# Optimization experiments

Measured on AMD Instinct MI355X. Metric: run time of the kernel, lower is better.

## Reference

```python
import jax, jax.numpy as jnp
import numpy as np


def setup_inputs() -> dict:
    key = jax.random.key(0)
    k1, k2, k3 = jax.random.split(key, 3)
    backbone_feature = jax.random.normal(k1, (8, 256), dtype=jnp.float32)
    grouping_result = jax.random.randint(k2, (8,), 0, 32, dtype=jnp.int64)
    feature = jax.random.normal(k3, (8, 32, 48, 48, 48), dtype=jnp.float32)
    return {"backbone_feature": backbone_feature,
            "grouping_result": grouping_result,
            "feature": feature}


def reference(backbone_feature, grouping_result, feature):
    # feature: [B, R, W, H, D]
    B, R, W, H, D = feature.shape
    dt = feature.dtype
    mgr = feature.mean()  # global mean over all samples/regions/voxels

    # --- per-region argmax position (first occurrence, matching strict '>' scan) ---
    flat = feature.reshape(B, R, W * H * D)
    am = jnp.argmax(flat, axis=-1)                      # [B, R]
    max_x = (am // (H * D)).astype(dt)                  # [B, R]
    max_y = ((am // D) % H).astype(dt)
    max_z = (am % D).astype(dt)

    i = jnp.arange(W, dtype=dt).reshape(1, 1, W, 1, 1)
    j = jnp.arange(H, dtype=dt).reshape(1, 1, 1, H, 1)
    k = jnp.arange(D, dtype=dt).reshape(1, 1, 1, 1, D)

    dx2 = (max_x[:, :, None, None, None] - i) ** 2      # [B,R,W,1,1]
    dy2 = (max_y[:, :, None, None, None] - j) ** 2      # [B,R,1,H,1]
    dz2 = (max_z[:, :, None, None, None] - k) ** 2      # [B,R,1,1,D]

    f2 = feature * feature
    # NOTE: faithful to original parenthesization: z-term is NOT weighted by region^2
    dis_loss = jnp.sum(f2 * (dx2 + dy2)) + jnp.sum(jnp.broadcast_to(dz2, (B, R, W, H, D)))

    # --- exclude-self max over regions via top-2 along region axis ---
    srt = jnp.sort(feature, axis=1)                     # ascending along R
    m1 = srt[:, -1]                                     # [B, W, H, D] max over regions
    m2 = srt[:, -2]                                     # second max
    argmax_r = jnp.argmax(feature, axis=1)              # [B, W, H, D] first-occurrence
    r_ids = jnp.arange(R).reshape(1, R, 1, 1, 1)
    max_others = jnp.where(r_ids == argmax_r[:, None], m2[:, None], m1[:, None])  # [B,R,W,H,D]

    div_loss = jnp.sum(f2 * (max_others - mgr) ** 2)

    sum_num = B * R * W * H * D
    return (jnp.reshape(dis_loss / sum_num, (1,)),
            jnp.reshape(div_loss / sum_num, (1,)))
```

## Files before the change

kernel.cpp:

```cpp
#include <hip/hip_runtime.h>
#include <math.h>

#define W48 48
#define HD 2304
#define WHD 110592
#define NR 32
#define NB 8
#define QPP 27648
#define CHUNKS 108
#define MAIN_BLOCKS 864
#define PARTS 432
#define NTOT 28311552.0

struct PPart { float s0, sx, sy; unsigned int fkey; unsigned int idx; };

__device__ __forceinline__ unsigned fkey_of(float f) {
  unsigned u = __float_as_uint(f);
  return (u & 0x80000000u) ? ~u : (u | 0x80000000u);
}

__device__ __forceinline__ float wave_red_add(float x) {
  int s;
  s = __builtin_amdgcn_update_dpp(0, __float_as_int(x), 0x111, 0xf, 0xf, true); x += __int_as_float(s);
  s = __builtin_amdgcn_update_dpp(0, __float_as_int(x), 0x112, 0xf, 0xf, true); x += __int_as_float(s);
  s = __builtin_amdgcn_update_dpp(0, __float_as_int(x), 0x114, 0xf, 0xf, true); x += __int_as_float(s);
  s = __builtin_amdgcn_update_dpp(0, __float_as_int(x), 0x118, 0xf, 0xf, true); x += __int_as_float(s);
  s = __builtin_amdgcn_update_dpp(0, __float_as_int(x), 0x142, 0xa, 0xf, true); x += __int_as_float(s);
  s = __builtin_amdgcn_update_dpp(0, __float_as_int(x), 0x143, 0xc, 0xf, true); x += __int_as_float(s);
  return x;
}
__device__ __forceinline__ unsigned wave_red_umax(unsigned x) {
  int s; unsigned u;
  s = __builtin_amdgcn_update_dpp(0, (int)x, 0x111, 0xf, 0xf, true); u = (unsigned)s; x = x > u ? x : u;
  s = __builtin_amdgcn_update_dpp(0, (int)x, 0x112, 0xf, 0xf, true); u = (unsigned)s; x = x > u ? x : u;
  s = __builtin_amdgcn_update_dpp(0, (int)x, 0x114, 0xf, 0xf, true); u = (unsigned)s; x = x > u ? x : u;
  s = __builtin_amdgcn_update_dpp(0, (int)x, 0x118, 0xf, 0xf, true); u = (unsigned)s; x = x > u ? x : u;
  s = __builtin_amdgcn_update_dpp(0, (int)x, 0x142, 0xa, 0xf, true); u = (unsigned)s; x = x > u ? x : u;
  s = __builtin_amdgcn_update_dpp(0, (int)x, 0x143, 0xc, 0xf, true); u = (unsigned)s; x = x > u ? x : u;
  return x;
}
__device__ __forceinline__ unsigned wave_red_umin(unsigned x) {
  int s; unsigned u;
  s = __builtin_amdgcn_update_dpp(-1, (int)x, 0x111, 0xf, 0xf, false); u = (unsigned)s; x = x < u ? x : u;
  s = __builtin_amdgcn_update_dpp(-1, (int)x, 0x112, 0xf, 0xf, false); u = (unsigned)s; x = x < u ? x : u;
  s = __builtin_amdgcn_update_dpp(-1, (int)x, 0x114, 0xf, 0xf, false); u = (unsigned)s; x = x < u ? x : u;
  s = __builtin_amdgcn_update_dpp(-1, (int)x, 0x118, 0xf, 0xf, false); u = (unsigned)s; x = x < u ? x : u;
  s = __builtin_amdgcn_update_dpp(-1, (int)x, 0x142, 0xa, 0xf, false); u = (unsigned)s; x = x < u ? x : u;
  s = __builtin_amdgcn_update_dpp(-1, (int)x, 0x143, 0xc, 0xf, false); u = (unsigned)s; x = x < u ? x : u;
  return x;
}

__global__ __launch_bounds__(256)
void k_main(const float* __restrict__ feat, PPart* __restrict__ pp,
            double* __restrict__ blk) {
  const int bid = blockIdx.x;
  const int t = threadIdx.x;
  const int b = bid / CHUNKS;
  const int chunk = bid - b * CHUNKS;
  const int qbase = chunk * 256 + t;
  const float4* gbase = reinterpret_cast<const float4*>(feat) + (size_t)b * (NR * QPP) + qbase;

  const int p0 = qbase * 4;
  const int i = p0 / HD;
  const int j = (p0 / W48) % W48;
  const float fi = (float)i, fj = (float)j;
  const float rr = fi * fi + fj * fj;

  const int wave = t >> 6, lane = t & 63;

  float v1[4], v2[4], cp[4];
#pragma unroll
  for (int c = 0; c < 4; ++c) { v1[c] = -INFINITY; v2[c] = -INFINITY; cp[c] = 0.f; }
  float ssum = 0.f, sii = 0.f;

  float4 b0 = gbase[0];
  float4 b1 = gbase[QPP];

#pragma unroll 2
  for (int r = 0; r < NR; ++r) {
    float4 v = b0;
    b0 = b1;
    if (r < NR - 2) b1 = gbase[(size_t)(r + 2) * QPP];

    float vv[4] = {v.x, v.y, v.z, v.w};
    float s0t = 0.f;
#pragma unroll
    for (int c = 0; c < 4; ++c) {
      float f = vv[c];
      float f2 = f * f;
      s0t += f2;
      cp[c] += f2;
      ssum += f;
      float nv2 = fmaxf(f, v2[c]);
      v2[c] = (f > v1[c]) ? v1[c] : nv2;
      v1[c] = fmaxf(v1[c], f);
    }
    float mv = vv[0]; int mc = 0;
#pragma unroll
    for (int c = 1; c < 4; ++c) { if (vv[c] > mv) { mv = vv[c]; mc = c; } }

    sii += s0t * rr;
    float rsx = wave_red_add(s0t * fi);
    float rsy = wave_red_add(s0t * fj);
    float rs0 = wave_red_add(s0t);
    unsigned key = fkey_of(mv);
    unsigned wmax = wave_red_umax(key);
    wmax = (unsigned)__builtin_amdgcn_readlane((int)wmax, 63);
    unsigned cand = (key == wmax) ? (unsigned)(p0 + mc) : 0xffffffffu;
    unsigned widx = wave_red_umin(cand);

    if (lane == 63) {
      PPart o; o.s0 = rs0; o.sx = rsx; o.sy = rsy; o.fkey = wmax; o.idx = widx;
      pp[((size_t)(b * NR + r) * CHUNKS + chunk) * 4 + wave] = o;
    }
  }

  float A = 0.f, Bs = 0.f, C = 0.f;
#pragma unroll
  for (int c = 0; c < 4; ++c) {
    float m1 = v1[c];
    float m1sq = m1 * m1;
    float rest = cp[c] - m1sq;
    A  += m1sq * rest + v2[c] * v2[c] * m1sq;
    Bs += m1 * rest + v2[c] * m1sq;
    C  += cp[c];
  }
  double dA = A, dB = Bs, dC = C, dS = ssum, dI = sii;
#pragma unroll
  for (int off = 32; off; off >>= 1) {
    dA += __shfl_down(dA, off);
    dB += __shfl_down(dB, off);
    dC += __shfl_down(dC, off);
    dS += __shfl_down(dS, off);
    dI += __shfl_down(dI, off);
  }
  __shared__ double ld[4][5];
  if (lane == 0) { ld[wave][0]=dA; ld[wave][1]=dB; ld[wave][2]=dC; ld[wave][3]=dS; ld[wave][4]=dI; }
  __syncthreads();
  if (t == 0) {
    double a=0, bb=0, cc=0, ss=0, si=0;
#pragma unroll
    for (int w = 0; w < 4; ++w) { a+=ld[w][0]; bb+=ld[w][1]; cc+=ld[w][2]; ss+=ld[w][3]; si+=ld[w][4]; }
    blk[(size_t)bid*5+0]=a; blk[(size_t)bid*5+1]=bb; blk[(size_t)bid*5+2]=cc;
    blk[(size_t)bid*5+3]=ss; blk[(size_t)bid*5+4]=si;
  }
}

__global__ __launch_bounds__(512)
void k_planes(const PPart* __restrict__ pp, double* __restrict__ planeDis) {
  const int p = blockIdx.x;
  const int t = threadIdx.x;
  double s0 = 0, sx = 0, sy = 0;
  unsigned fkey = 0, idx = 0xffffffffu;
  if (t < PARTS) {
    PPart v = pp[(size_t)p * PARTS + t];
    s0 = v.s0; sx = v.sx; sy = v.sy; fkey = v.fkey; idx = v.idx;
  }
#pragma unroll
  for (int off = 32; off; off >>= 1) {
    s0 += __shfl_down(s0, off);
    sx += __shfl_down(sx, off);
    sy += __shfl_down(sy, off);
    unsigned ok = __shfl_down(fkey, off);
    unsigned oi = __shfl_down(idx, off);
    if (ok > fkey || (ok == fkey && oi < idx)) { fkey = ok; idx = oi; }
  }
  __shared__ double ls[8][3];
  __shared__ unsigned lk[8][2];
  const int wave = t >> 6, lane = t & 63;
  if (lane == 0) { ls[wave][0]=s0; ls[wave][1]=sx; ls[wave][2]=sy; lk[wave][0]=fkey; lk[wave][1]=idx; }
  __syncthreads();
  if (t == 0) {
    double a0=0, a1=0, a2=0; unsigned bk=0, bi=0xffffffffu;
#pragma unroll
    for (int w = 0; w < 8; ++w) {
      a0 += ls[w][0]; a1 += ls[w][1]; a2 += ls[w][2];
      if (lk[w][0] > bk || (lk[w][0]==bk && lk[w][1] < bi)) { bk = lk[w][0]; bi = lk[w][1]; }
    }
    int am = (int)bi;
    int mx = am / HD;
    int rem = am - mx * HD;
    int my = rem / W48;
    int mz = rem - my * W48;
    double dmx = mx, dmy = my, dmz = mz;
    planeDis[p] = (dmx*dmx + dmy*dmy) * a0 - 2.0*dmx*a1 - 2.0*dmy*a2
                + 2304.0 * (48.0*dmz*dmz - 2256.0*dmz + 35720.0);
  }
}

__global__ __launch_bounds__(256)
void k_fin(const double* __restrict__ planeDis, const double* __restrict__ blk,
           float* __restrict__ out) {
  const int t = threadIdx.x;
  double dis = planeDis[t];
  double A = 0, B = 0, C = 0, S = 0, SII = 0;
  for (int i = t; i < MAIN_BLOCKS; i += 256) {
    A   += blk[(size_t)i*5+0];
    B   += blk[(size_t)i*5+1];
    C   += blk[(size_t)i*5+2];
    S   += blk[(size_t)i*5+3];
    SII += blk[(size_t)i*5+4];
  }
#pragma unroll
  for (int off = 32; off; off >>= 1) {
    dis += __shfl_down(dis, off);
    A   += __shfl_down(A, off);
    B   += __shfl_down(B, off);
    C   += __shfl_down(C, off);
    S   += __shfl_down(S, off);
    SII += __shfl_down(SII, off);
  }
  __shared__ double ls[4][6];
  const int wave = t >> 6, lane = t & 63;
  if (lane == 0) {
    ls[wave][0]=dis; ls[wave][1]=A; ls[wave][2]=B; ls[wave][3]=C; ls[wave][4]=S; ls[wave][5]=SII;
  }
  __syncthreads();
  if (t == 0) {
    double td=0, tA=0, tB=0, tC=0, tS=0, tI=0;
#pragma unroll
    for (int w = 0; w < 4; ++w) {
      td+=ls[w][0]; tA+=ls[w][1]; tB+=ls[w][2]; tC+=ls[w][3]; tS+=ls[w][4]; tI+=ls[w][5];
    }
    double mgr = tS / NTOT;
    out[0] = (float)((td + tI) / NTOT);
    out[1] = (float)((tA - 2.0*mgr*tB + mgr*mgr*tC) / NTOT);
  }
}

extern "C" void kernel_launch(void* const* d_in, const int* in_sizes, int n_in,
                              void* d_out, int out_size, void* d_ws, size_t ws_size,
                              hipStream_t stream) {
  const float* feat = (const float*)d_in[2];
  float* out = (float*)d_out;

  PPart* pp = (PPart*)d_ws;
  double* blk = (double*)((char*)d_ws + 2211840);
  double* planeDis = (double*)((char*)d_ws + 2211840 + 34560);

  k_main<<<MAIN_BLOCKS, 256, 0, stream>>>(feat, pp, blk);
  k_planes<<<256, 512, 0, stream>>>(pp, planeDis);
  k_fin<<<1, 256, 0, stream>>>(planeDis, blk, out);
}
```

Before: 43.63 us.

## Replace per-region DPP wave reductions with batched LDS transpose reduction

Instead of running five DPP wave reductions for every region in every wave, each thread stores its per-region sum of squares and argmax key into LDS. Every 16 regions the block transposes and reduces them, so each thread handles one region over 16 rows. Per-block partials drop from four per wave to one per chunk, which shrinks the partial buffer and lets k_planes use 128-thread blocks. In exchange it uses about 36KB of LDS, which can lower occupancy, and adds barriers inside the fully unrolled region loop.

```diff
diff --git a/kernel.cpp b/kernel.cpp
--- a/kernel.cpp
+++ b/kernel.cpp
@@ -9,123 +9,127 @@
 #define QPP 27648
 #define CHUNKS 108
 #define MAIN_BLOCKS 864
-#define PARTS 432
 #define NTOT 28311552.0
 
-struct PPart { float s0, sx, sy; unsigned int fkey; unsigned int idx; };
-
-__device__ __forceinline__ unsigned fkey_of(float f) {
-  unsigned u = __float_as_uint(f);
-  return (u & 0x80000000u) ? ~u : (u | 0x80000000u);
-}
-
-__device__ __forceinline__ float wave_red_add(float x) {
-  int s;
-  s = __builtin_amdgcn_update_dpp(0, __float_as_int(x), 0x111, 0xf, 0xf, true); x += __int_as_float(s);
-  s = __builtin_amdgcn_update_dpp(0, __float_as_int(x), 0x112, 0xf, 0xf, true); x += __int_as_float(s);
-  s = __builtin_amdgcn_update_dpp(0, __float_as_int(x), 0x114, 0xf, 0xf, true); x += __int_as_float(s);
-  s = __builtin_amdgcn_update_dpp(0, __float_as_int(x), 0x118, 0xf, 0xf, true); x += __int_as_float(s);
-  s = __builtin_amdgcn_update_dpp(0, __float_as_int(x), 0x142, 0xa, 0xf, true); x += __int_as_float(s);
-  s = __builtin_amdgcn_update_dpp(0, __float_as_int(x), 0x143, 0xc, 0xf, true); x += __int_as_float(s);
-  return x;
-}
-__device__ __forceinline__ unsigned wave_red_umax(unsigned x) {
-  int s; unsigned u;
-  s = __builtin_amdgcn_update_dpp(0, (int)x, 0x111, 0xf, 0xf, true); u = (unsigned)s; x = x > u ? x : u;
-  s = __builtin_amdgcn_update_dpp(0, (int)x, 0x112, 0xf, 0xf, true); u = (unsigned)s; x = x > u ? x : u;
-  s = __builtin_amdgcn_update_dpp(0, (int)x, 0x114, 0xf, 0xf, true); u = (unsigned)s; x = x > u ? x : u;
-  s = __builtin_amdgcn_update_dpp(0, (int)x, 0x118, 0xf, 0xf, true); u = (unsigned)s; x = x > u ? x : u;
-  s = __builtin_amdgcn_update_dpp(0, (int)x, 0x142, 0xa, 0xf, true); u = (unsigned)s; x = x > u ? x : u;
-  s = __builtin_amdgcn_update_dpp(0, (int)x, 0x143, 0xc, 0xf, true); u = (unsigned)s; x = x > u ? x : u;
-  return x;
-}
-__device__ __forceinline__ unsigned wave_red_umin(unsigned x) {
-  int s; unsigned u;
-  s = __builtin_amdgcn_update_dpp(-1, (int)x, 0x111, 0xf, 0xf, false); u = (unsigned)s; x = x < u ? x : u;
-  s = __builtin_amdgcn_update_dpp(-1, (int)x, 0x112, 0xf, 0xf, false); u = (unsigned)s; x = x < u ? x : u;
-  s = __builtin_amdgcn_update_dpp(-1, (int)x, 0x114, 0xf, 0xf, false); u = (unsigned)s; x = x < u ? x : u;
-  s = __builtin_amdgcn_update_dpp(-1, (int)x, 0x118, 0xf, 0xf, false); u = (unsigned)s; x = x < u ? x : u;
-  s = __builtin_amdgcn_update_dpp(-1, (int)x, 0x142, 0xa, 0xf, false); u = (unsigned)s; x = x < u ? x : u;
-  s = __builtin_amdgcn_update_dpp(-1, (int)x, 0x143, 0xc, 0xf, false); u = (unsigned)s; x = x < u ? x : u;
-  return x;
-}
+struct PPart { float s0, sx, sy; unsigned key; unsigned idx; };
 
 __global__ __launch_bounds__(256)
 void k_main(const float* __restrict__ feat, PPart* __restrict__ pp,
             double* __restrict__ blk) {
+  __shared__ float    lds_s0[16 * 256];
+  __shared__ unsigned lds_key[16 * 256];
+  __shared__ unsigned lds_mc[256];
+  __shared__ float comb_s0[256], comb_sx[256], comb_sy[256];
+  __shared__ unsigned comb_key[256], comb_idx[256];
+  __shared__ double ld[4][5];
+
   const int bid = blockIdx.x;
   const int t = threadIdx.x;
   const int b = bid / CHUNKS;
   const int chunk = bid - b * CHUNKS;
   const int qbase = chunk * 256 + t;
-  const float4* gbase = reinterpret_cast<const float4*>(feat) + (size_t)b * (NR * QPP) + qbase;
+  const float4* gptr = reinterpret_cast<const float4*>(feat) + (size_t)b * (NR * QPP) + qbase;
 
   const int p0 = qbase * 4;
-  const int i = p0 / HD;
-  const int j = (p0 / W48) % W48;
-  const float fi = (float)i, fj = (float)j;
-  const float rr = fi * fi + fj * fj;
-
-  const int wave = t >> 6, lane = t & 63;
+  const float fi = (float)(p0 / HD);
+  const float fj = (float)((p0 / W48) % W48);
+  const float rrq = fi * fi + fj * fj;
 
   float v1[4], v2[4], cp[4];
 #pragma unroll
   for (int c = 0; c < 4; ++c) { v1[c] = -INFINITY; v2[c] = -INFINITY; cp[c] = 0.f; }
   float ssum = 0.f, sii = 0.f;
-
-  float4 b0 = gbase[0];
-  float4 b1 = gbase[QPP];
-
-#pragma unroll 2
+  unsigned mcpack = 0u;
+
+  float4 nb0 = gptr[0];
+  float4 nb1 = gptr[QPP];
+
+#pragma unroll
   for (int r = 0; r < NR; ++r) {
-    float4 v = b0;
-    b0 = b1;
-    if (r < NR - 2) b1 = gbase[(size_t)(r + 2) * QPP];
+    float4 v = nb0; nb0 = nb1;
+    if (r < NR - 2) nb1 = gptr[(size_t)(r + 2) * QPP];
 
     float vv[4] = {v.x, v.y, v.z, v.w};
-    float s0t = 0.f;
+    float f2[4];
 #pragma unroll
     for (int c = 0; c < 4; ++c) {
       float f = vv[c];
-      float f2 = f * f;
-      s0t += f2;
-      cp[c] += f2;
+      f2[c] = f * f;
+      cp[c] += f2[c];
       ssum += f;
       float nv2 = fmaxf(f, v2[c]);
       v2[c] = (f > v1[c]) ? v1[c] : nv2;
       v1[c] = fmaxf(v1[c], f);
     }
+    float s0t = (f2[0] + f2[1]) + (f2[2] + f2[3]);
+    sii += s0t * rrq;
+
     float mv = vv[0]; int mc = 0;
 #pragma unroll
     for (int c = 1; c < 4; ++c) { if (vv[c] > mv) { mv = vv[c]; mc = c; } }
-
-    sii += s0t * rr;
-    float rsx = wave_red_add(s0t * fi);
-    float rsy = wave_red_add(s0t * fj);
-    float rs0 = wave_red_add(s0t);
-    unsigned key = fkey_of(mv);
-    unsigned wmax = wave_red_umax(key);
-    wmax = (unsigned)__builtin_amdgcn_readlane((int)wmax, 63);
-    unsigned cand = (key == wmax) ? (unsigned)(p0 + mc) : 0xffffffffu;
-    unsigned widx = wave_red_umin(cand);
-
-    if (lane == 63) {
-      PPart o; o.s0 = rs0; o.sx = rsx; o.sy = rsy; o.fkey = wmax; o.idx = widx;
-      pp[((size_t)(b * NR + r) * CHUNKS + chunk) * 4 + wave] = o;
+    unsigned u = __float_as_uint(mv);
+    unsigned key = u ^ ((unsigned)((int)u >> 31) | 0x80000000u);
+
+    const int r16 = r & 15;
+    mcpack |= (unsigned)mc << (2 * r16);
+    lds_s0[r16 * 256 + t] = s0t;
+    lds_key[r16 * 256 + t] = key;
+
+    if (r16 == 15) {
+      lds_mc[t] = mcpack; mcpack = 0u;
+      __syncthreads();
+      const int half = r >> 4;
+      const int er = t & 15;
+      const int eg = t >> 4;
+      float es0 = 0.f, esx = 0.f, esy = 0.f;
+      unsigned bk = 0u; int brow = 0;
+#pragma unroll
+      for (int k = 0; k < 16; ++k) {
+        int row = eg * 16 + ((k + er) & 15);
+        float s0v   = lds_s0[er * 256 + row];
+        unsigned kv = lds_key[er * 256 + row];
+        unsigned q = (unsigned)(chunk * 256 + row);
+        float fiq = (float)(q / 576u);
+        float fjq = (float)((q / 12u) % 48u);
+        es0 += s0v;
+        esx = fmaf(s0v, fiq, esx);
+        esy = fmaf(s0v, fjq, esy);
+        if (kv > bk || (kv == bk && row < brow)) { bk = kv; brow = row; }
+      }
+      unsigned wmc = (lds_mc[brow] >> (2 * er)) & 3u;
+      unsigned bidx = (unsigned)((chunk * 256 + brow) * 4) + wmc;
+      __syncthreads();
+      comb_s0[t] = es0; comb_sx[t] = esx; comb_sy[t] = esy;
+      comb_key[t] = bk; comb_idx[t] = bidx;
+      __syncthreads();
+      if (t < 16) {
+        float ps0 = 0.f, psx = 0.f, psy = 0.f;
+        unsigned fk = 0u, fidx = 0xffffffffu;
+#pragma unroll
+        for (int g2 = 0; g2 < 16; ++g2) {
+          int ii = g2 * 16 + t;
+          ps0 += comb_s0[ii]; psx += comb_sx[ii]; psy += comb_sy[ii];
+          unsigned ck = comb_key[ii], ci = comb_idx[ii];
+          if (ck > fk || (ck == fk && ci < fidx)) { fk = ck; fidx = ci; }
+        }
+        int plane = b * NR + half * 16 + t;
+        PPart o; o.s0 = ps0; o.sx = psx; o.sy = psy; o.key = fk; o.idx = fidx;
+        pp[(size_t)plane * CHUNKS + chunk] = o;
+      }
     }
   }
 
   float A = 0.f, Bs = 0.f, C = 0.f;
 #pragma unroll
   for (int c = 0; c < 4; ++c) {
-    float m1 = v1[c];
-    float m1sq = m1 * m1;
+    float m1 = v1[c], m1sq = m1 * m1;
     float rest = cp[c] - m1sq;
     A  += m1sq * rest + v2[c] * v2[c] * m1sq;
     Bs += m1 * rest + v2[c] * m1sq;
     C  += cp[c];
   }
   double dA = A, dB = Bs, dC = C, dS = ssum, dI = sii;
+  const int wave = t >> 6, lane = t & 63;
 #pragma unroll
   for (int off = 32; off; off >>= 1) {
     dA += __shfl_down(dA, off);
@@ -134,7 +138,6 @@
     dS += __shfl_down(dS, off);
     dI += __shfl_down(dI, off);
   }
-  __shared__ double ld[4][5];
   if (lane == 0) { ld[wave][0]=dA; ld[wave][1]=dB; ld[wave][2]=dC; ld[wave][3]=dS; ld[wave][4]=dI; }
   __syncthreads();
   if (t == 0) {
@@ -146,15 +149,15 @@
   }
 }
 
-__global__ __launch_bounds__(512)
+__global__ __launch_bounds__(128)
 void k_planes(const PPart* __restrict__ pp, double* __restrict__ planeDis) {
   const int p = blockIdx.x;
   const int t = threadIdx.x;
   double s0 = 0, sx = 0, sy = 0;
   unsigned fkey = 0, idx = 0xffffffffu;
-  if (t < PARTS) {
-    PPart v = pp[(size_t)p * PARTS + t];
-    s0 = v.s0; sx = v.sx; sy = v.sy; fkey = v.fkey; idx = v.idx;
+  if (t < CHUNKS) {
+    PPart v = pp[(size_t)p * CHUNKS + t];
+    s0 = v.s0; sx = v.sx; sy = v.sy; fkey = v.key; idx = v.idx;
   }
 #pragma unroll
   for (int off = 32; off; off >>= 1) {
@@ -165,15 +168,15 @@
     unsigned oi = __shfl_down(idx, off);
     if (ok > fkey || (ok == fkey && oi < idx)) { fkey = ok; idx = oi; }
   }
-  __shared__ double ls[8][3];
-  __shared__ unsigned lk[8][2];
+  __shared__ double ls[2][3];
+  __shared__ unsigned lk[2][2];
   const int wave = t >> 6, lane = t & 63;
   if (lane == 0) { ls[wave][0]=s0; ls[wave][1]=sx; ls[wave][2]=sy; lk[wave][0]=fkey; lk[wave][1]=idx; }
   __syncthreads();
   if (t == 0) {
     double a0=0, a1=0, a2=0; unsigned bk=0, bi=0xffffffffu;
 #pragma unroll
-    for (int w = 0; w < 8; ++w) {
+    for (int w = 0; w < 2; ++w) {
       a0 += ls[w][0]; a1 += ls[w][1]; a2 += ls[w][2];
       if (lk[w][0] > bk || (lk[w][0]==bk && lk[w][1] < bi)) { bk = lk[w][0]; bi = lk[w][1]; }
     }
@@ -235,10 +238,10 @@
   float* out = (float*)d_out;
 
   PPart* pp = (PPart*)d_ws;
-  double* blk = (double*)((char*)d_ws + 2211840);
-  double* planeDis = (double*)((char*)d_ws + 2211840 + 34560);
+  double* blk = (double*)((char*)d_ws + 552960);
+  double* planeDis = (double*)((char*)d_ws + 552960 + 34560);
 
   k_main<<<MAIN_BLOCKS, 256, 0, stream>>>(feat, pp, blk);
-  k_planes<<<256, 512, 0, stream>>>(pp, planeDis);
+  k_planes<<<256, 128, 0, stream>>>(pp, planeDis);
   k_fin<<<1, 256, 0, stream>>>(planeDis, blk, out);
 }
```

Result: slower. 58.12 us (+33.2%).
